# Kernel tuning notes

Hardware: AMD Instinct MI355X
Metric: run time of the kernel (lower is better)

The kernel has to match this reference:

```python
import jax, jax.numpy as jnp
import numpy as np

DIM = 256
HEADS = 8
HEAD_DIM = 32
INNER = HEADS * HEAD_DIM  # 256
B, L_AG, H, W = 2, 5, 32, 32
SEQ = H * W
POS_HID = 32


def _lin(k, fan_in, fan_out):
    kw, kb = jax.random.split(k)
    Wt = jax.random.normal(kw, (fan_in, fan_out), jnp.float32) * (fan_in ** -0.5)
    b = jax.random.normal(kb, (fan_out,), jnp.float32) * 0.01
    return Wt, b


def setup_inputs() -> dict:
    key = jax.random.key(0)
    ks = jax.random.split(key, 10)
    x = jax.random.normal(ks[0], (B, L_AG, H, W, DIM), jnp.float32)
    Wq, bq = _lin(ks[1], DIM, INNER)
    Wk, bk = _lin(ks[2], DIM, INNER)
    Wv, bv = _lin(ks[3], DIM, INNER)
    Wp1, bp1 = _lin(ks[4], 3, POS_HID)
    Wp2, bp2 = _lin(ks[5], POS_HID, HEADS)
    Ws1, bs1 = _lin(ks[6], DIM, POS_HID)
    Ws2, bs2 = _lin(ks[7], POS_HID, HEADS)
    Wo, bo = _lin(ks[8], INNER, DIM)
    Wg, bg = _lin(ks[9], 2 * DIM, DIM)
    return dict(x=x, Wq=Wq, bq=bq, Wk=Wk, bk=bk, Wv=Wv, bv=bv,
                Wp1=Wp1, bp1=bp1, Wp2=Wp2, bp2=bp2,
                Ws1=Ws1, bs1=bs1, Ws2=Ws2, bs2=bs2,
                Wo=Wo, bo=bo, Wg=Wg, bg=bg)


def _relative_positions(h, w):
    # coords: (h*w, 2), row-major (i//w, i%w) like torch meshgrid 'ij'
    yy, xx = jnp.meshgrid(jnp.arange(h), jnp.arange(w), indexing='ij')
    coords = jnp.stack([yy.reshape(-1), xx.reshape(-1)], axis=-1)  # (L,2)
    rel = (coords[:, None, :] - coords[None, :, :]).astype(jnp.float32)  # (L,L,2)
    dist = jnp.linalg.norm(rel, axis=-1, keepdims=True)  # (L,L,1)
    return jnp.concatenate([rel, dist], axis=-1)  # (L,L,3)


def reference(x, Wq, bq, Wk, bk, Wv, bv, Wp1, bp1, Wp2, bp2,
              Ws1, bs1, Ws2, bs2, Wo, bo, Wg, bg):
    b, l, h, w, c = x.shape
    bl, L = b * l, h * w
    scale = HEAD_DIM ** -0.5
    x2 = x.reshape(bl, L, c)

    q = (x2 @ Wq + bq).reshape(bl, L, HEADS, HEAD_DIM)
    k = (x2 @ Wk + bk).reshape(bl, L, HEADS, HEAD_DIM)
    v = (x2 @ Wv + bv).reshape(bl, L, HEADS, HEAD_DIM)

    scores = jnp.einsum('bihd,bjhd->bhij', q, k) * scale  # (bl,H,L,L)

    rel_pos = _relative_positions(h, w)  # (L,L,3)
    pos_w = jax.nn.relu(rel_pos @ Wp1 + bp1) @ Wp2 + bp2  # (L,L,heads)
    pos_w = jnp.transpose(pos_w, (2, 0, 1))[None]  # (1,heads,L,L)

    s = jax.nn.relu(x2 @ Ws1 + bs1) @ Ws2 + bs2  # (bl,L,heads)
    fsim = jnp.einsum('bih,bjh->bij', s, s)[:, None]  # (bl,1,L,L)

    probs = jax.nn.softmax(scores + pos_w + fsim, axis=-1)
    out = jnp.einsum('bhij,bjhd->bihd', probs, v).reshape(bl, L, INNER)
    out = out @ Wo + bo  # (bl,L,dim); dropout is identity in eval

    gate = jax.nn.sigmoid(jnp.concatenate([x2, out], axis=-1) @ Wg + bg)
    out = gate * out + (1.0 - gate) * x2
    return out.reshape(b, l, h, w, c)
```

## Files before the change

### kernel.cpp

```cpp
#include <hip/hip_runtime.h>

typedef __bf16 bf16_t;
typedef __bf16 bf16x4 __attribute__((ext_vector_type(4)));
typedef __bf16 bf16x8 __attribute__((ext_vector_type(8)));
typedef float  f32x4  __attribute__((ext_vector_type(4)));

#define HEADS 8
#define HEAD_DIM 32
#define DIM 256
#define BL 10
#define SEQ 1024
#define M_TOTAL (BL*SEQ)
#define QK_SCALE 0.17677669529663687f
#define LOG2E 1.4426950408889634f
#define SQRT_LOG2E 1.2011224087864498f
#define NPOS (63*63)

#define NCAST 2596
#define NTRANS 96
#define NPREP (NCAST + NTRANS + 16)

__device__ __forceinline__ int swz_idx(int row, int col) {
  return row*64 + (col ^ ((row & 7) << 3));
}
__device__ __forceinline__ int swzk(int row, int col) {
  return row*32 + (col ^ (((row >> 1) & 3) << 3));
}
__device__ __forceinline__ int swz256(int row, int col) {
  return row*256 + (col ^ ((row & 7) << 3));
}

__global__ __launch_bounds__(256) void prep_all_kernel(
    const float* __restrict__ x, const float* __restrict__ Ws1,
    const float* __restrict__ bq, const float* __restrict__ bk,
    const float* __restrict__ bv, const float* __restrict__ bs1,
    const float* __restrict__ Wq, const float* __restrict__ Wk, const float* __restrict__ Wv,
    const float* __restrict__ Wo, const float* __restrict__ Wg,
    const float* __restrict__ Wp1, const float* __restrict__ bp1,
    const float* __restrict__ Wp2, const float* __restrict__ bp2,
    bf16_t* __restrict__ xb, bf16_t* __restrict__ btall, float* __restrict__ bias_all,
    bf16_t* __restrict__ wot, bf16_t* __restrict__ wg1t, bf16_t* __restrict__ wg2t,
    float* __restrict__ posT)
{
  __shared__ float tile[64][65];
  const int bid = blockIdx.x;
  const int tid = threadIdx.x;

  if (bid < NCAST) {
    const int NX4 = M_TOTAL*DIM/4;
    const int i = bid*256 + tid;
    if (i < NX4) {
      const float4 v = ((const float4*)x)[i];
      bf16x4 o; o[0]=(bf16_t)v.x; o[1]=(bf16_t)v.y; o[2]=(bf16_t)v.z; o[3]=(bf16_t)v.w;
      *(bf16x4*)(xb + (size_t)i*4) = o;
      return;
    }
    int idx = i - NX4;
    if (idx < 8192) {
      const int m = idx >> 8, k = idx & 255;
      btall[(768 + m)*256 + k] = (bf16_t)Ws1[k*32 + m];
      return;
    }
    idx -= 8192;
    if (idx < 832) {
      bias_all[idx] = (idx < 256) ? bq[idx] : (idx < 512) ? bk[idx-256] :
                      (idx < 768) ? bv[idx-512] : (idx < 800) ? bs1[idx-768] : 0.f;
    }
    return;
  }

  if (bid < NCAST + NTRANS) {
    const int t0 = bid - NCAST;
    const int z = t0 >> 4, bi = (t0 & 15) >> 2, bj = t0 & 3;
    const float* src; bf16_t* dst;
    switch (z) {
      case 0: src = Wq;          dst = btall;          break;
      case 1: src = Wk;          dst = btall + 65536;  break;
      case 2: src = Wv;          dst = btall + 131072; break;
      case 3: src = Wo;          dst = wot;            break;
      case 4: src = Wg;          dst = wg1t;           break;
      default: src = Wg + 65536; dst = wg2t;           break;
    }
    const int tr = tid >> 4, tc = tid & 15;
    #pragma unroll
    for (int i = 0; i < 4; ++i) {
      const float4 v = *(const float4*)(src + (size_t)(bi*64 + tr + 16*i)*256 + bj*64 + tc*4);
      float* tp = &tile[tr + 16*i][tc*4];
      tp[0]=v.x; tp[1]=v.y; tp[2]=v.z; tp[3]=v.w;
    }
    __syncthreads();
    #pragma unroll
    for (int i = 0; i < 4; ++i) {
      bf16x4 o;
      #pragma unroll
      for (int e = 0; e < 4; ++e) o[e] = (bf16_t)tile[tc*4 + e][tr + 16*i];
      *(bf16x4*)(dst + (size_t)(bj*64 + tr + 16*i)*256 + bi*64 + tc*4) = o;
    }
    return;
  }

  {
    float* sm = &tile[0][0];
    float* w1 = sm; float* b1 = sm + 96; float* w2 = sm + 128; float* b2 = sm + 384;
    if (tid < 96) w1[tid] = Wp1[tid];
    if (tid < 32) b1[tid] = bp1[tid];
    w2[tid] = Wp2[tid];
    if (tid < 8)  b2[tid] = bp2[tid];
    __syncthreads();
    const int p = (bid - NCAST - NTRANS)*256 + tid;
    if (p >= NPOS) return;
    const float dy = (float)(p / 63 - 31);
    const float dx = (float)(p % 63 - 31);
    const float dist = sqrtf(dy*dy + dx*dx);
    float o[8];
    #pragma unroll
    for (int t = 0; t < 8; ++t) o[t] = b2[t];
    #pragma unroll
    for (int m = 0; m < 32; ++m) {
      float hv = fmaf(dy, w1[m], fmaf(dx, w1[32+m], fmaf(dist, w1[64+m], b1[m])));
      hv = fmaxf(hv, 0.f);
      #pragma unroll
      for (int t = 0; t < 8; ++t) o[t] = fmaf(hv, w2[m*8+t], o[t]);
    }
    #pragma unroll
    for (int t = 0; t < 8; ++t) posT[t*NPOS + p] = o[t]*LOG2E;
  }
}

__global__ __launch_bounds__(256) void qkv_kernel(
    const bf16_t* __restrict__ xb, const bf16_t* __restrict__ btall,
    const float* __restrict__ bias_all, const float* __restrict__ Ws2,
    const float* __restrict__ bs2,
    bf16_t* __restrict__ qbuf, bf16_t* __restrict__ kbuf, bf16_t* __restrict__ vbuf,
    bf16_t* __restrict__ sbb)
{
  __shared__ float hidlds[64][33];
  const int mt = blockIdx.x, ngb = blockIdx.y;
  const int tid = threadIdx.x;
  const int w = tid >> 6, lane = tid & 63, g = lane >> 4, l15 = lane & 15;
  const int arow = mt*64 + w*16 + l15;
  const bf16x8* Arow = (const bf16x8*)(xb + (size_t)arow*DIM);
  bf16x8 af[8];
  #pragma unroll
  for (int kc = 0; kc < 8; ++kc) af[kc] = Arow[kc*4 + g];
  if (ngb < 12) {
    bf16_t* dst = (ngb < 4) ? qbuf : (ngb < 8) ? kbuf : vbuf;
    const int coloff = (ngb & 3) * 64;
    const float scale = (ngb < 4) ? QK_SCALE*LOG2E : 1.f;
    for (int c = 0; c < 4; ++c) {
      const int n = ngb*64 + c*16 + l15;
      const bf16x8* Brow = (const bf16x8*)(btall + (size_t)n*DIM);
      f32x4 acc = {0.f,0.f,0.f,0.f};
      #pragma unroll
      for (int kc = 0; kc < 8; ++kc)
        acc = __builtin_amdgcn_mfma_f32_16x16x32_bf16(af[kc], Brow[kc*4+g], acc, 0, 0, 0);
      const float bvv = bias_all[n];
      #pragma unroll
      for (int r = 0; r < 4; ++r) {
        const int row = mt*64 + w*16 + g*4 + r;
        dst[(size_t)row*DIM + coloff + c*16 + l15] = (bf16_t)((acc[r] + bvv)*scale);
      }
    }
  } else {
    for (int c = 0; c < 2; ++c) {
      const int n = 768 + c*16 + l15;
      const bf16x8* Brow = (const bf16x8*)(btall + (size_t)n*DIM);
      f32x4 acc = {0.f,0.f,0.f,0.f};
      #pragma unroll
      for (int kc = 0; kc < 8; ++kc)
        acc = __builtin_amdgcn_mfma_f32_16x16x32_bf16(af[kc], Brow[kc*4+g], acc, 0, 0, 0);
      const float bvv = bias_all[n];
      #pragma unroll
      for (int r = 0; r < 4; ++r)
        hidlds[w*16 + g*4 + r][c*16 + l15] = fmaxf(acc[r] + bvv, 0.f);
    }
    __syncthreads();
    if (tid < 64) {
      float sv[8];
      #pragma unroll
      for (int t = 0; t < 8; ++t) sv[t] = bs2[t];
      #pragma unroll
      for (int m = 0; m < 32; ++m) {
        const float hv = hidlds[tid][m];
        #pragma unroll
        for (int t = 0; t < 8; ++t) sv[t] = fmaf(hv, Ws2[m*8+t], sv[t]);
      }
      bf16x8 o;
      #pragma unroll
      for (int t = 0; t < 8; ++t) o[t] = (bf16_t)(sv[t]*SQRT_LOG2E);
      *(bf16x8*)(sbb + (size_t)(mt*64 + tid)*8) = o;
    }
  }
}

__global__ __launch_bounds__(256) void attn_kernel(
    const bf16_t* __restrict__ qb, const bf16_t* __restrict__ kb,
    const bf16_t* __restrict__ vb, const bf16_t* __restrict__ sbb,
    const float* __restrict__ posT, bf16_t* __restrict__ att)
{
  __shared__ __align__(16) bf16_t lk[2][64*32];
  __shared__ __align__(16) bf16_t ls[2][64*8];
  __shared__ __align__(16) bf16_t lv[2][32*64];
  __shared__ __align__(16) bf16_t lp[64*64];
  __shared__ float ptab[33*63];

  const int wg = blockIdx.x;
  const int xcd = wg & 7, within = wg >> 3;
  const int pair = xcd*10 + (within >> 4);
  const int it = within & 15;
  const int h = pair & 7, b = pair >> 3;
  const int i0 = it*64, iy0 = it*2;
  const int tid = threadIdx.x;
  const int w = tid >> 6, lane = tid & 63, g = lane >> 4, l15 = lane & 15;
  const int r4 = tid >> 2, q4 = tid & 3;

  for (int p = tid; p < 33*63; p += 256) {
    const int rr = p / 63, cc = p - rr*63;
    ptab[p] = posT[h*NPOS + (iy0 + rr)*63 + cc];
  }

  const int qrow = b*SEQ + i0 + w*16 + l15;
  const bf16x8 aq0 = *(const bf16x8*)(qb + (size_t)qrow*DIM + h*HEAD_DIM + g*8);
  bf16x8 aq1 = {};
  if (g == 0) aq1 = *(const bf16x8*)(sbb + (size_t)qrow*8);

  const int iq = i0 + w*16 + l15;
  const int rbase_i = (iq >> 5) - iy0 + 31;
  const int ixr = iq & 31;

  int paddr[16];
  #pragma unroll
  for (int c = 0; c < 4; ++c) {
    #pragma unroll
    for (int r = 0; r < 4; ++r) {
      const int jl = c*16 + g*4 + r;
      paddr[c*4+r] = ((rbase_i - (jl >> 5))*63 + (ixr - (jl & 31) + 31)) * 4;
    }
  }

  bf16x8 kreg = *(const bf16x8*)(kb + (size_t)(b*SEQ + r4)*DIM + h*HEAD_DIM + q4*8);
  bf16x8 vreg = *(const bf16x8*)(vb + (size_t)(b*SEQ + r4)*DIM + h*HEAD_DIM + q4*8);
  bf16x8 sreg = {};
  if (tid < 64) sreg = *(const bf16x8*)(sbb + (size_t)(b*SEQ + tid)*8);
  *(bf16x8*)&lk[0][swzk(r4, q4*8)] = kreg;
  #pragma unroll
  for (int e = 0; e < 8; ++e) {
    const int d = q4*8 + e;
    lv[0][d*64 + (r4 ^ ((d & 7) << 3))] = vreg[e];
  }
  if (tid < 64) *(bf16x8*)&ls[0][tid*8] = sreg;
  __syncthreads();

  f32x4 accO0 = {0.f,0.f,0.f,0.f}, accO1 = {0.f,0.f,0.f,0.f};
  float mrow = -1e30f, lrow = 0.f;

  for (int jt = 0; jt < 16; ++jt) {
    const int pb = jt & 1;
    if (jt < 15) {
      const int grow = b*SEQ + jt*64 + 64;
      kreg = *(const bf16x8*)(kb + (size_t)(grow + r4)*DIM + h*HEAD_DIM + q4*8);
      vreg = *(const bf16x8*)(vb + (size_t)(grow + r4)*DIM + h*HEAD_DIM + q4*8);
      if (tid < 64) sreg = *(const bf16x8*)(sbb + (size_t)(grow + tid)*8);
    }

    f32x4 s4[4];
    #pragma unroll
    for (int c = 0; c < 4; ++c) {
      const bf16x8 kf0 = *(const bf16x8*)&lk[pb][swzk(c*16 + l15, g*8)];
      bf16x8 kf1 = {};
      if (g == 0) kf1 = *(const bf16x8*)&ls[pb][(c*16 + l15)*8];
      f32x4 acc = {0.f,0.f,0.f,0.f};
      acc = __builtin_amdgcn_mfma_f32_16x16x32_bf16(kf0, aq0, acc, 0, 0, 0);
      acc = __builtin_amdgcn_mfma_f32_16x16x32_bf16(kf1, aq1, acc, 0, 0, 0);
      s4[c] = acc;
    }

    #pragma unroll
    for (int c = 0; c < 4; ++c) {
      #pragma unroll
      for (int r = 0; r < 4; ++r) {
        s4[c][r] += *(const float*)((const char*)ptab + paddr[c*4+r]);
        paddr[c*4+r] -= 504;
      }
    }

    float m16 = s4[0][0];
    #pragma unroll
    for (int c = 0; c < 4; ++c) {
      #pragma unroll
      for (int r = 0; r < 4; ++r) m16 = fmaxf(m16, s4[c][r]);
    }
    m16 = fmaxf(m16, __shfl_xor(m16, 16));
    m16 = fmaxf(m16, __shfl_xor(m16, 32));
    if (__any(m16 > mrow + 8.f)) {
      const float mn = fmaxf(mrow, m16);
      const float alpha = exp2f(mrow - mn);
      mrow = mn;
      lrow *= alpha;
      #pragma unroll
      for (int r = 0; r < 4; ++r) {
        const float aO = __shfl(alpha, g*16 + g*4 + r);
        accO0[r] *= aO; accO1[r] *= aO;
      }
    }
    float rsum = 0.f;
    #pragma unroll
    for (int c = 0; c < 4; ++c) {
      #pragma unroll
      for (int r = 0; r < 4; ++r) {
        s4[c][r] = exp2f(s4[c][r] - mrow);
        rsum += s4[c][r];
      }
    }
    lrow += rsum;

    #pragma unroll
    for (int c = 0; c < 4; ++c) {
      bf16x4 o;
      #pragma unroll
      for (int r = 0; r < 4; ++r) o[r] = (bf16_t)s4[c][r];
      *(bf16x4*)&lp[swz_idx(w*16 + l15, c*16 + g*4)] = o;
    }

    const int prow = w*16 + l15;
    #pragma unroll
    for (int kc = 0; kc < 2; ++kc) {
      const bf16x8 ap  = *(const bf16x8*)&lp[swz_idx(prow, kc*32 + g*8)];
      const bf16x8 bv0 = *(const bf16x8*)&lv[pb][swz_idx(l15,      kc*32 + g*8)];
      const bf16x8 bv1 = *(const bf16x8*)&lv[pb][swz_idx(16 + l15, kc*32 + g*8)];
      accO0 = __builtin_amdgcn_mfma_f32_16x16x32_bf16(ap, bv0, accO0, 0, 0, 0);
      accO1 = __builtin_amdgcn_mfma_f32_16x16x32_bf16(ap, bv1, accO1, 0, 0, 0);
    }

    if (jt < 15) {
      *(bf16x8*)&lk[pb^1][swzk(r4, q4*8)] = kreg;
      #pragma unroll
      for (int e = 0; e < 8; ++e) {
        const int d = q4*8 + e;
        lv[pb^1][d*64 + (r4 ^ ((d & 7) << 3))] = vreg[e];
      }
      if (tid < 64) *(bf16x8*)&ls[pb^1][tid*8] = sreg;
    }
    __syncthreads();
  }

  lrow += __shfl_xor(lrow, 16);
  lrow += __shfl_xor(lrow, 32);
  #pragma unroll
  for (int r = 0; r < 4; ++r) {
    const int row = b*SEQ + i0 + w*16 + g*4 + r;
    const float inv = 1.f / __shfl(lrow, g*16 + g*4 + r);
    att[(size_t)row*DIM + h*HEAD_DIM + l15]      = (bf16_t)(accO0[r]*inv);
    att[(size_t)row*DIM + h*HEAD_DIM + 16 + l15] = (bf16_t)(accO1[r]*inv);
  }
}

__global__ __launch_bounds__(256) void prjgate_kernel(
    const bf16_t* __restrict__ att, const bf16_t* __restrict__ wot,
    const float* __restrict__ bo, const bf16_t* __restrict__ xb,
    const float* __restrict__ x, const bf16_t* __restrict__ wg1t,
    const bf16_t* __restrict__ wg2t, const float* __restrict__ bg,
    float* __restrict__ outp)
{
  __shared__ __align__(16) bf16_t prjT[16*256];
  const int row0 = blockIdx.x * 16;
  const int tid = threadIdx.x;
  const int w = tid >> 6, lane = tid & 63, g = lane >> 4, l15 = lane & 15;
  const int arow = row0 + l15;

  {
    const bf16x8* Arow = (const bf16x8*)(att + (size_t)arow*DIM);
    bf16x8 afA[8];
    #pragma unroll
    for (int kc = 0; kc < 8; ++kc) afA[kc] = Arow[kc*4 + g];
    #pragma unroll
    for (int ct = 0; ct < 4; ++ct) {
      const int n = w*64 + ct*16 + l15;
      const bf16x8* Brow = (const bf16x8*)(wot + (size_t)n*DIM);
      f32x4 acc = {0.f,0.f,0.f,0.f};
      #pragma unroll
      for (int kc = 0; kc < 8; ++kc)
        acc = __builtin_amdgcn_mfma_f32_16x16x32_bf16(afA[kc], Brow[kc*4+g], acc, 0, 0, 0);
      const float bvo = bo[n];
      #pragma unroll
      for (int r = 0; r < 4; ++r)
        prjT[swz256(g*4 + r, n)] = (bf16_t)(acc[r] + bvo);
    }
  }
  __syncthreads();

  const bf16x8* A1r = (const bf16x8*)(xb + (size_t)arow*DIM);
  bf16x8 a1[8], a2[8];
  #pragma unroll
  for (int kc = 0; kc < 8; ++kc) {
    a1[kc] = A1r[kc*4 + g];
    a2[kc] = *(const bf16x8*)&prjT[swz256(l15, kc*32 + g*8)];
  }
  #pragma unroll
  for (int ct = 0; ct < 4; ++ct) {
    const int n = w*64 + ct*16 + l15;
    const bf16x8* b1 = (const bf16x8*)(wg1t + (size_t)n*DIM);
    const bf16x8* b2 = (const bf16x8*)(wg2t + (size_t)n*DIM);
    f32x4 acc = {0.f,0.f,0.f,0.f};
    #pragma unroll
    for (int kc = 0; kc < 8; ++kc)
      acc = __builtin_amdgcn_mfma_f32_16x16x32_bf16(a1[kc], b1[kc*4+g], acc, 0, 0, 0);
    #pragma unroll
    for (int kc = 0; kc < 8; ++kc)
      acc = __builtin_amdgcn_mfma_f32_16x16x32_bf16(a2[kc], b2[kc*4+g], acc, 0, 0, 0);
    const float bgv = bg[n];
    #pragma unroll
    for (int r = 0; r < 4; ++r) {
      const int grow = row0 + g*4 + r;
      const float gate = 1.f / (1.f + __expf(-(acc[r] + bgv)));
      const float pv = (float)prjT[swz256(g*4 + r, n)];
      const float xv = x[(size_t)grow*DIM + n];
      outp[(size_t)grow*DIM + n] = gate*pv + (1.f - gate)*xv;
    }
  }
}

extern "C" void kernel_launch(void* const* d_in, const int* in_sizes, int n_in,
                              void* d_out, int out_size, void* d_ws, size_t ws_size,
                              hipStream_t stream)
{
  const float* x   = (const float*)d_in[0];
  const float* Wq  = (const float*)d_in[1];
  const float* bq  = (const float*)d_in[2];
  const float* Wk  = (const float*)d_in[3];
  const float* bk  = (const float*)d_in[4];
  const float* Wv  = (const float*)d_in[5];
  const float* bv  = (const float*)d_in[6];
  const float* Wp1 = (const float*)d_in[7];
  const float* bp1 = (const float*)d_in[8];
  const float* Wp2 = (const float*)d_in[9];
  const float* bp2 = (const float*)d_in[10];
  const float* Ws1 = (const float*)d_in[11];
  const float* bs1 = (const float*)d_in[12];
  const float* Ws2 = (const float*)d_in[13];
  const float* bs2 = (const float*)d_in[14];
  const float* Wo  = (const float*)d_in[15];
  const float* bo  = (const float*)d_in[16];
  const float* Wg  = (const float*)d_in[17];
  const float* bg  = (const float*)d_in[18];

  char* ws = (char*)d_ws;
  size_t off = 0;
  auto alloc = [&](size_t bytes) {
    char* p = ws + off;
    off += (bytes + 255) & ~(size_t)255;
    return p;
  };
  bf16_t* xb    = (bf16_t*)alloc((size_t)M_TOTAL*DIM*2);
  bf16_t* qbuf  = (bf16_t*)alloc((size_t)M_TOTAL*DIM*2);
  bf16_t* kbuf  = (bf16_t*)alloc((size_t)M_TOTAL*DIM*2);
  bf16_t* vbuf  = (bf16_t*)alloc((size_t)M_TOTAL*DIM*2);
  bf16_t* att   = (bf16_t*)alloc((size_t)M_TOTAL*DIM*2);
  bf16_t* btall = (bf16_t*)alloc((size_t)800*256*2);
  bf16_t* wot   = (bf16_t*)alloc(65536*2);
  bf16_t* wg1t  = (bf16_t*)alloc(65536*2);
  bf16_t* wg2t  = (bf16_t*)alloc(65536*2);
  float*  bias_all = (float*)alloc(832*4);
  bf16_t* sbb   = (bf16_t*)alloc((size_t)M_TOTAL*8*2);
  float*  posT  = (float*)alloc((size_t)HEADS*NPOS*4);
  (void)ws_size; (void)in_sizes; (void)n_in; (void)out_size;

  prep_all_kernel<<<NPREP, 256, 0, stream>>>(x, Ws1, bq, bk, bv, bs1,
                                             Wq, Wk, Wv, Wo, Wg, Wp1, bp1, Wp2, bp2,
                                             xb, btall, bias_all, wot, wg1t, wg2t, posT);
  qkv_kernel<<<dim3(M_TOTAL/64, 13), 256, 0, stream>>>(xb, btall, bias_all, Ws2, bs2,
                                                       qbuf, kbuf, vbuf, sbb);
  attn_kernel<<<SEQ/64*HEADS*BL, 256, 0, stream>>>(qbuf, kbuf, vbuf, sbb, posT, att);
  prjgate_kernel<<<M_TOTAL/16, 256, 0, stream>>>(att, wot, bo, xb, x, wg1t, wg2t, bg,
                                                 (float*)d_out);
}
```

Measured before the change: 173.8 us.

## Remap workgroups per XCD and use a reversed, padded position-bias table

The qkv and projection/gate kernels now remap the flat workgroup index so that consecutive row tiles land on the same XCD. This is meant to improve L2 locality for the shared A rows, and the qkv grid becomes 1D. In the attention kernel, the relative-position table is stored column-reversed with a row pitch of 64. Per-tile addresses are then computed from a contiguous base plus r, which removes the 16-register address array and its per-iteration updates. The trade is a slightly larger LDS table, extra index arithmetic, and remapping code that hard-codes the grid sizes.

```diff
diff --git a/kernel.cpp b/kernel.cpp
--- a/kernel.cpp
+++ b/kernel.cpp
@@ -135,7 +135,10 @@
     bf16_t* __restrict__ sbb)
 {
   __shared__ float hidlds[64][33];
-  const int mt = blockIdx.x, ngb = blockIdx.y;
+  const int wg = blockIdx.x;
+  const int xcd = wg & 7, within = wg >> 3;
+  const int mt = xcd*20 + within/13;
+  const int ngb = within - (within/13)*13;
   const int tid = threadIdx.x;
   const int w = tid >> 6, lane = tid & 63, g = lane >> 4, l15 = lane & 15;
   const int arow = mt*64 + w*16 + l15;
@@ -202,7 +205,7 @@
   __shared__ __align__(16) bf16_t ls[2][64*8];
   __shared__ __align__(16) bf16_t lv[2][32*64];
   __shared__ __align__(16) bf16_t lp[64*64];
-  __shared__ float ptab[33*63];
+  __shared__ float ptabR[33*64];
 
   const int wg = blockIdx.x;
   const int xcd = wg & 7, within = wg >> 3;
@@ -214,9 +217,9 @@
   const int w = tid >> 6, lane = tid & 63, g = lane >> 4, l15 = lane & 15;
   const int r4 = tid >> 2, q4 = tid & 3;
 
-  for (int p = tid; p < 33*63; p += 256) {
-    const int rr = p / 63, cc = p - rr*63;
-    ptab[p] = posT[h*NPOS + (iy0 + rr)*63 + cc];
+  for (int p = tid; p < 33*64; p += 256) {
+    const int rr = p >> 6, cR = p & 63;
+    ptabR[p] = (cR < 63) ? posT[h*NPOS + (iy0 + rr)*63 + (62 - cR)] : 0.f;
   }
 
   const int qrow = b*SEQ + i0 + w*16 + l15;
@@ -226,17 +229,7 @@
 
   const int iq = i0 + w*16 + l15;
   const int rbase_i = (iq >> 5) - iy0 + 31;
-  const int ixr = iq & 31;
-
-  int paddr[16];
-  #pragma unroll
-  for (int c = 0; c < 4; ++c) {
-    #pragma unroll
-    for (int r = 0; r < 4; ++r) {
-      const int jl = c*16 + g*4 + r;
-      paddr[c*4+r] = ((rbase_i - (jl >> 5))*63 + (ixr - (jl & 31) + 31)) * 4;
-    }
-  }
+  const int xbase = 31 - (iq & 31);
 
   bf16x8 kreg = *(const bf16x8*)(kb + (size_t)(b*SEQ + r4)*DIM + h*HEAD_DIM + q4*8);
   bf16x8 vreg = *(const bf16x8*)(vb + (size_t)(b*SEQ + r4)*DIM + h*HEAD_DIM + q4*8);
@@ -277,11 +270,10 @@
 
     #pragma unroll
     for (int c = 0; c < 4; ++c) {
-      #pragma unroll
-      for (int r = 0; r < 4; ++r) {
-        s4[c][r] += *(const float*)((const char*)ptab + paddr[c*4+r]);
-        paddr[c*4+r] -= 504;
-      }
+      const int prowi = (rbase_i - jt*2 - (c >> 1))*64 + xbase + (c & 1)*16 + g*4;
+      #pragma unroll
+      for (int r = 0; r < 4; ++r)
+        s4[c][r] += ptabR[prowi + r];
     }
 
     float m16 = s4[0][0];
@@ -363,7 +355,8 @@
     float* __restrict__ outp)
 {
   __shared__ __align__(16) bf16_t prjT[16*256];
-  const int row0 = blockIdx.x * 16;
+  const int wg = blockIdx.x;
+  const int row0 = ((wg & 7)*80 + (wg >> 3)) * 16;
   const int tid = threadIdx.x;
   const int w = tid >> 6, lane = tid & 63, g = lane >> 4, l15 = lane & 15;
   const int arow = row0 + l15;
@@ -468,9 +461,9 @@
   prep_all_kernel<<<NPREP, 256, 0, stream>>>(x, Ws1, bq, bk, bv, bs1,
                                              Wq, Wk, Wv, Wo, Wg, Wp1, bp1, Wp2, bp2,
                                              xb, btall, bias_all, wot, wg1t, wg2t, posT);
-  qkv_kernel<<<dim3(M_TOTAL/64, 13), 256, 0, stream>>>(xb, btall, bias_all, Ws2, bs2,
-                                                       qbuf, kbuf, vbuf, sbb);
+  qkv_kernel<<<2080, 256, 0, stream>>>(xb, btall, bias_all, Ws2, bs2,
+                                       qbuf, kbuf, vbuf, sbb);
   attn_kernel<<<SEQ/64*HEADS*BL, 256, 0, stream>>>(qbuf, kbuf, vbuf, sbb, posT, att);
-  prjgate_kernel<<<M_TOTAL/16, 256, 0, stream>>>(att, wot, bo, xb, x, wg1t, wg2t, bg,
-                                                 (float*)d_out);
-}
+  prjgate_kernel<<<640, 256, 0, stream>>>(att, wot, bo, xb, x, wg1t, wg2t, bg,
+                                          (float*)d_out);
+}
```

New measurement: 151.3 us. 1.15x faster.
